# Optimization experiments

Hardware: AMD Instinct MI355X
Metric: run time of the kernel (lower is better)

## Reference

```python
import jax, jax.numpy as jnp
import numpy as np

D_MODEL = 2048
N_HEADS = 16
D_HEAD = D_MODEL // N_HEADS
SQLEN = 2048
EPS = 1e-5
XPOS_SCALE_BASE = 512.0


def apply_xpos(x, offset, inv=False):
    # x: (sqlen, d_head). Rotary embedding with xPos exponential length scaling.
    sqlen, d = x.shape
    half = d // 2
    freq = 1.0 / (10000.0 ** (jnp.arange(half, dtype=jnp.float32) / half))
    pos = jnp.arange(sqlen, dtype=jnp.float32) + offset  # absolute positions
    ang = pos[:, None] * freq[None, :]                   # (sqlen, half)
    sin, cos = jnp.sin(ang), jnp.cos(ang)
    # xPos per-dim scale zeta^(pos/scale_base); k gets the inverse scale.
    zeta = (jnp.arange(half, dtype=jnp.float32) * 2.0 + 0.4 * d) / (1.4 * d)
    sc = zeta[None, :] ** (pos[:, None] / XPOS_SCALE_BASE)
    if inv:
        sc = 1.0 / sc
    x1, x2 = x[:, :half], x[:, half:]
    r1 = (x1 * cos - x2 * sin) * sc
    r2 = (x2 * cos + x1 * sin) * sc
    return jnp.concatenate([r1, r2], axis=-1)


def group_norm(x, weight, bias):
    # x: (sqlen, d_model); n_heads groups of d_head channels each.
    xg = x.reshape(x.shape[0], N_HEADS, D_HEAD)
    mu = jnp.mean(xg, axis=-1, keepdims=True)
    var = jnp.mean((xg - mu) ** 2, axis=-1, keepdims=True)
    xn = ((xg - mu) * jax.lax.rsqrt(var + EPS)).reshape(x.shape)
    return xn * weight + bias


def setup_inputs() -> dict:
    key = jax.random.key(0)
    ks = jax.random.split(key, 9)
    s = 0.02
    return {
        "x": jax.random.normal(ks[0], (SQLEN, D_MODEL), dtype=jnp.float32),
        "state": jax.random.normal(ks[1], (N_HEADS, D_HEAD, D_HEAD), dtype=jnp.float32),
        "W_qkv": jax.random.normal(ks[2], (3 * D_MODEL, D_MODEL), dtype=jnp.float32) * s,
        "W_alpha": jax.random.normal(ks[3], (N_HEADS, D_MODEL), dtype=jnp.float32) * s,
        "b_alpha": jnp.zeros((N_HEADS,), dtype=jnp.float32),
        "alpha_base": jnp.log(jax.random.uniform(ks[4], (N_HEADS,), minval=0.95, maxval=0.999)).astype(jnp.float32),
        "gn_weight": jnp.ones((D_MODEL,), dtype=jnp.float32),
        "gn_bias": jnp.zeros((D_MODEL,), dtype=jnp.float32),
        "W_out": jax.random.normal(ks[5], (D_MODEL, D_MODEL), dtype=jnp.float32) * s,
        "W_gate": jax.random.normal(ks[6], (D_MODEL, D_MODEL), dtype=jnp.float32) * s,
        "offset": 0,
    }


def reference(x, state, W_qkv, W_alpha, b_alpha, alpha_base, gn_weight, gn_bias, W_out, W_gate, offset):
    sqlen = x.shape[0]
    # qkv projection -> (3, h, sqlen, d_head)
    qkv = (x @ W_qkv.T).reshape(sqlen, 3, N_HEADS, D_HEAD).transpose(1, 2, 0, 3)
    q, k, v = qkv[0], qkv[1], qkv[2]
    q = jax.vmap(lambda t: apply_xpos(t, offset))(q)
    k = jax.vmap(lambda t: apply_xpos(t, offset, inv=True))(k)

    # per-head, per-position decay log-rates: (h, sqlen), negative
    alphas = jax.nn.sigmoid(x @ W_alpha.T + b_alpha).T
    alphas = alpha_base[:, None] * 8.0 * alphas
    k = (1.0 - jnp.exp(alphas))[:, :, None] * k
    alphas = jnp.cumsum(alphas, axis=1)
    # causal decay matrix Delta[h,i,j] = exp(a_i - a_j) for j <= i
    Delta = jnp.tril(jnp.exp(alphas[:, :, None] - alphas[:, None, :]))

    attn = jnp.einsum('hid,hjd,hij->hij', q, k, Delta)
    ret = jnp.einsum('hij,hje->ihe', attn, v)  # (sqlen, h, d_head)

    # recurrent state carry
    new_state = jnp.exp(alphas[:, -1, None, None]) * state
    ret = ret + jnp.einsum('hid,hde,hi->ihe', q, state, jnp.exp(alphas))
    new_state = new_state + jnp.einsum('hid,hie,hi->hde', k, v, Delta[:, -1, :])

    ret = ret.reshape(sqlen, D_MODEL)
    ret = group_norm(ret, gn_weight, gn_bias)
    out = (jax.nn.swish(ret @ W_gate.T) * ret) @ W_out.T
    return (out, new_state)
```

## Files before the change

kernel.cpp:

```cpp
#include <hip/hip_runtime.h>
#include <cstddef>

#define SQLEN 2048
#define DMODEL 2048
#define NHEADS 16
#define DHEAD 128

typedef __attribute__((ext_vector_type(8))) short bf16x8;
typedef __attribute__((ext_vector_type(4))) float floatx4;

__device__ __forceinline__ unsigned short f2bf(float f) {
  union { float f; unsigned u; } c; c.f = f;
  unsigned u = c.u;
  unsigned r = u + 0x7fffu + ((u >> 16) & 1u);
  return (unsigned short)(r >> 16);
}
__device__ __forceinline__ float bf2f(unsigned short s) {
  union { unsigned u; float f; } c; c.u = ((unsigned)s) << 16;
  return c.f;
}

__global__ __launch_bounds__(256) void f2b_kernel(const float4* __restrict__ in,
                                                  ushort4* __restrict__ out) {
  int i = blockIdx.x * 256 + threadIdx.x;
  float4 v = in[i];
  ushort4 o;
  o.x = f2bf(v.x); o.y = f2bf(v.y); o.z = f2bf(v.z); o.w = f2bf(v.w);
  out[i] = o;
}

__global__ __launch_bounds__(256) void gemm_bf16_nt(const unsigned short* __restrict__ A,
                                                    const unsigned short* __restrict__ B,
                                                    float* __restrict__ C,
                                                    int M, int N, int K) {
  __shared__ __align__(16) unsigned short As[128 * 32];
  __shared__ __align__(16) unsigned short Bs[128 * 32];
  int tid = threadIdx.x;
  int wave = tid >> 6;
  int lane = tid & 63;
  int wm = wave >> 1, wn = wave & 1;
  int quad = lane >> 4, m16 = lane & 15;
  int row0 = blockIdx.y * 128, col0 = blockIdx.x * 128;

  floatx4 acc[4][4];
#pragma unroll
  for (int i = 0; i < 4; i++)
#pragma unroll
    for (int j = 0; j < 4; j++) acc[i][j] = (floatx4){0.f, 0.f, 0.f, 0.f};

  int c0 = tid, c1 = tid + 256;
  int r0c = c0 >> 2, q0c = (c0 & 3) * 8;
  int r1c = c1 >> 2, q1c = (c1 & 3) * 8;

  const size_t sK = (size_t)K;
  for (int k0 = 0; k0 < K; k0 += 32) {
    __builtin_amdgcn_global_load_lds(
        (const __attribute__((address_space(1))) unsigned int*)(A + (size_t)(row0 + r0c) * sK + k0 + q0c),
        (__attribute__((address_space(3))) unsigned int*)(As + c0 * 8), 16, 0, 0);
    __builtin_amdgcn_global_load_lds(
        (const __attribute__((address_space(1))) unsigned int*)(A + (size_t)(row0 + r1c) * sK + k0 + q1c),
        (__attribute__((address_space(3))) unsigned int*)(As + c1 * 8), 16, 0, 0);
    __builtin_amdgcn_global_load_lds(
        (const __attribute__((address_space(1))) unsigned int*)(B + (size_t)(col0 + r0c) * sK + k0 + q0c),
        (__attribute__((address_space(3))) unsigned int*)(Bs + c0 * 8), 16, 0, 0);
    __builtin_amdgcn_global_load_lds(
        (const __attribute__((address_space(1))) unsigned int*)(B + (size_t)(col0 + r1c) * sK + k0 + q1c),
        (__attribute__((address_space(3))) unsigned int*)(Bs + c1 * 8), 16, 0, 0);
    __syncthreads();

    bf16x8 af[4], bfr[4];
#pragma unroll
    for (int i = 0; i < 4; i++)
      af[i] = *(const bf16x8*)(As + (wm * 64 + i * 16 + m16) * 32 + quad * 8);
#pragma unroll
    for (int j = 0; j < 4; j++)
      bfr[j] = *(const bf16x8*)(Bs + (wn * 64 + j * 16 + m16) * 32 + quad * 8);
#pragma unroll
    for (int i = 0; i < 4; i++)
#pragma unroll
      for (int j = 0; j < 4; j++)
        acc[i][j] = __builtin_amdgcn_mfma_f32_16x16x32_bf16(af[i], bfr[j], acc[i][j], 0, 0, 0);
    __syncthreads();
  }

#pragma unroll
  for (int i = 0; i < 4; i++) {
#pragma unroll
    for (int j = 0; j < 4; j++) {
      int rr = row0 + wm * 64 + i * 16 + quad * 4;
      int cc = col0 + wn * 64 + j * 16 + m16;
#pragma unroll
      for (int r = 0; r < 4; r++)
        C[(size_t)(rr + r) * N + cc] = acc[i][j][r];
    }
  }
}

__global__ __launch_bounds__(256) void alpha_kernel(const float* __restrict__ x,
                                                    const float* __restrict__ W_alpha,
                                                    const float* __restrict__ b_alpha,
                                                    const float* __restrict__ alpha_base,
                                                    float* __restrict__ a_raw) {
  __shared__ float xs[4][2048];
  int tid = threadIdx.x;
  int t0 = blockIdx.x * 4;
#pragma unroll
  for (int p = 0; p < 8; p++) {
    int idx = tid + p * 256;
    int row = idx >> 9, c4 = idx & 511;
    *(float4*)&xs[row][c4 * 4] = *(const float4*)(x + (size_t)(t0 + row) * DMODEL + c4 * 4);
  }
  __syncthreads();
  int w = tid >> 6, lane = tid & 63;
  int t = t0 + w;
#pragma unroll
  for (int h = 0; h < NHEADS; h++) {
    const float4* wr = (const float4*)(W_alpha + (size_t)h * DMODEL);
    float s = 0.f;
#pragma unroll
    for (int i = lane; i < 512; i += 64) {
      float4 a = *(const float4*)&xs[w][i * 4];
      float4 b = wr[i];
      s += a.x * b.x + a.y * b.y + a.z * b.z + a.w * b.w;
    }
#pragma unroll
    for (int off = 32; off > 0; off >>= 1) s += __shfl_down(s, off);
    if (lane == 0) {
      float sig = 1.f / (1.f + expf(-(s + b_alpha[h])));
      a_raw[(size_t)h * SQLEN + t] = alpha_base[h] * 8.f * sig;
    }
  }
}

__global__ __launch_bounds__(256) void cumsum_kernel(const float* __restrict__ a_raw,
                                                     float* __restrict__ A) {
  int h = blockIdx.x;
  __shared__ float part[256];
  int tid = threadIdx.x;
  float v[8];
  float s = 0.f;
#pragma unroll
  for (int i = 0; i < 8; i++) {
    v[i] = a_raw[(size_t)h * SQLEN + tid * 8 + i];
    s += v[i];
  }
  part[tid] = s;
  __syncthreads();
  for (int off = 1; off < 256; off <<= 1) {
    float tmp = (tid >= off) ? part[tid - off] : 0.f;
    __syncthreads();
    part[tid] += tmp;
    __syncthreads();
  }
  float run = (tid > 0) ? part[tid - 1] : 0.f;
#pragma unroll
  for (int i = 0; i < 8; i++) {
    run += v[i];
    A[(size_t)h * SQLEN + tid * 8 + i] = run;
  }
}

__global__ __launch_bounds__(256) void xpos_kernel(const float* __restrict__ qkv,
                                                   const float* __restrict__ a_raw,
                                                   const int* __restrict__ offset_p,
                                                   unsigned short* __restrict__ qb,
                                                   unsigned short* __restrict__ kb,
                                                   unsigned short* __restrict__ vb) {
  int idx = blockIdx.x * 256 + threadIdx.x;
  int j = idx & 63;
  int t = (idx >> 6) & 2047;
  int h = idx >> 17;
  float pos = (float)(t + offset_p[0]);
  float freq = exp2f(-(float)j * (13.287712379549449f / 64.f));
  float ang = pos * freq;
  float sn = sinf(ang), cs = cosf(ang);
  float zeta = (2.f * (float)j + 51.2f) / 179.2f;
  float lzp = log2f(zeta) * pos * (1.f / 512.f);
  float sc = exp2f(lzp);
  float sci = exp2f(-lzp);
  const float* row = qkv + (size_t)t * (3 * DMODEL);
  int base = h * DHEAD + j;
  float q1 = row[base], q2 = row[base + 64];
  float k1 = row[DMODEL + base], k2 = row[DMODEL + base + 64];
  float v1 = row[2 * DMODEL + base], v2 = row[2 * DMODEL + base + 64];
  size_t o = ((size_t)h * SQLEN + t) * DHEAD + j;
  qb[o] = f2bf((q1 * cs - q2 * sn) * sc);
  qb[o + 64] = f2bf((q2 * cs + q1 * sn) * sc);
  float km = (1.f - expf(a_raw[(size_t)h * SQLEN + t])) * sci;
  kb[o] = f2bf((k1 * cs - k2 * sn) * km);
  kb[o + 64] = f2bf((k2 * cs + k1 * sn) * km);
  vb[o] = f2bf(v1);
  vb[o + 64] = f2bf(v2);
}

__global__ __launch_bounds__(256) void transpose_kv_kernel(const unsigned short* __restrict__ kb,
                                                           const unsigned short* __restrict__ vb,
                                                           const float* __restrict__ A,
                                                           unsigned short* __restrict__ kT,
                                                           unsigned short* __restrict__ vT) {
  __shared__ __align__(16) unsigned short tile[64][72];
  int h = blockIdx.z >> 1, sel = blockIdx.z & 1;
  int t0 = blockIdx.x * 64, d0 = blockIdx.y * 64;
  int tid = threadIdx.x;
  const unsigned short* src = (sel ? vb : kb) + ((size_t)h * SQLEN + t0) * DHEAD + d0;
  unsigned short* dst = (sel ? vT : kT) + (size_t)h * (DHEAD * SQLEN) + (size_t)d0 * SQLEN + t0;
  float B = A[(size_t)h * SQLEN + SQLEN - 1];
#pragma unroll
  for (int p = 0; p < 2; p++) {
    int c = tid + p * 256;
    int r = c >> 3, off = (c & 7) * 8;
    bf16x8 in = *(const bf16x8*)(src + (size_t)r * DHEAD + off);
    if (!sel) {
      float w = __expf(B - A[(size_t)h * SQLEN + t0 + r]);
      bf16x8 o;
#pragma unroll
      for (int j = 0; j < 8; j++) o[j] = (short)f2bf(bf2f((unsigned short)in[j]) * w);
      *(bf16x8*)&tile[r][off] = o;
    } else {
      *(bf16x8*)&tile[r][off] = in;
    }
  }
  __syncthreads();
#pragma unroll
  for (int p = 0; p < 2; p++) {
    int c = tid + p * 256;
    int dr = c >> 3, toff = (c & 7) * 8;
    bf16x8 o;
#pragma unroll
    for (int j = 0; j < 8; j++) o[j] = (short)tile[toff + j][dr];
    *(bf16x8*)(dst + (size_t)dr * SQLEN + toff) = o;
  }
}

__global__ __launch_bounds__(256) void transpose_state_kernel(const float* __restrict__ st,
                                                              unsigned short* __restrict__ stT) {
  __shared__ float tile[64][65];
  int h = blockIdx.z, d0 = blockIdx.x * 64, e0 = blockIdx.y * 64;
  int tid = threadIdx.x;
  const float* src = st + (size_t)h * 16384 + (size_t)d0 * DHEAD + e0;
#pragma unroll
  for (int p = 0; p < 4; p++) {
    int idx = tid + p * 256;
    int r = idx >> 4, c = (idx & 15) * 4;
    float4 f = *(const float4*)(src + (size_t)r * DHEAD + c);
    tile[r][c] = f.x; tile[r][c + 1] = f.y; tile[r][c + 2] = f.z; tile[r][c + 3] = f.w;
  }
  __syncthreads();
  unsigned short* dst = stT + (size_t)h * 16384 + (size_t)e0 * DHEAD + d0;
#pragma unroll
  for (int p = 0; p < 2; p++) {
    int idx = tid + p * 256;
    int er = idx >> 3, doff = (idx & 7) * 8;
    bf16x8 o;
#pragma unroll
    for (int j = 0; j < 8; j++) o[j] = (short)f2bf(tile[doff + j][er]);
    *(bf16x8*)(dst + (size_t)er * DHEAD + doff) = o;
  }
}

__global__ __launch_bounds__(256) void retention_mfma(const unsigned short* __restrict__ qb,
                                                      const unsigned short* __restrict__ kb,
                                                      const unsigned short* __restrict__ vT,
                                                      const unsigned short* __restrict__ stT,
                                                      const float* __restrict__ A,
                                                      float* __restrict__ ret) {
  __shared__ __align__(16) unsigned short qs[64 * 128];
  __shared__ __align__(16) unsigned short ks[64 * 128];
  __shared__ __align__(16) unsigned short vs[128 * 64];
  __shared__ __align__(16) unsigned short Ss[64 * 72];
  __shared__ float djs[64];
  int h = blockIdx.x;
  int i0 = blockIdx.y * 64;
  int tid = threadIdx.x;
  int wave = tid >> 6, lane = tid & 63, quad = lane >> 4, m16 = lane & 15;
  const float* Ah = A + (size_t)h * SQLEN;
  float c = Ah[i0];

  const unsigned short* qh = qb + ((size_t)h * SQLEN + i0) * DHEAD;
#pragma unroll
  for (int p = 0; p < 4; p++) {
    int cch = tid + p * 256;
    int r = cch >> 4, kp = (cch & 15) ^ (r & 7);
    __builtin_amdgcn_global_load_lds(
        (const __attribute__((address_space(1))) unsigned int*)(qh + (size_t)r * DHEAD + kp * 8),
        (__attribute__((address_space(3))) unsigned int*)(qs + cch * 8), 16, 0, 0);
  }
  __syncthreads();

  int rq = wave * 16 + m16;
  bf16x8 qf[4];
#pragma unroll
  for (int dc = 0; dc < 4; dc++)
    qf[dc] = *(const bf16x8*)(qs + rq * 128 + (((dc * 4 + quad) ^ (rq & 7)) * 8));
  float ei = __expf(Ah[i0 + rq] - c);

  floatx4 acc[8];
#pragma unroll
  for (int et = 0; et < 8; et++) acc[et] = (floatx4){0.f, 0.f, 0.f, 0.f};

  if (c > -87.f) {
    const unsigned short* sp = stT + (size_t)h * 16384;
    float ecr[4];
#pragma unroll
    for (int r = 0; r < 4; r++) ecr[r] = __expf(Ah[i0 + wave * 16 + quad * 4 + r]);
#pragma unroll
    for (int et = 0; et < 8; et++) {
#pragma unroll
      for (int dc = 0; dc < 4; dc++) {
        bf16x8 sf = *(const bf16x8*)(sp + (et * 16 + m16) * DHEAD + dc * 32 + quad * 8);
        acc[et] = __builtin_amdgcn_mfma_f32_16x16x32_bf16(qf[dc], sf, acc[et], 0, 0, 0);
      }
#pragma unroll
      for (int r = 0; r < 4; r++) acc[et][r] *= ecr[r];
    }
  }

  for (int j0 = 0; j0 <= i0; j0 += 64) {
    if (c - Ah[j0 + 63] < -87.f) continue;
    __syncthreads();
    const unsigned short* kh = kb + ((size_t)h * SQLEN + j0) * DHEAD;
    const unsigned short* vh = vT + (size_t)h * (DHEAD * SQLEN) + j0;
#pragma unroll
    for (int p = 0; p < 4; p++) {
      int cch = tid + p * 256;
      int r = cch >> 4, kp = (cch & 15) ^ (r & 7);
      __builtin_amdgcn_global_load_lds(
          (const __attribute__((address_space(1))) unsigned int*)(kh + (size_t)r * DHEAD + kp * 8),
          (__attribute__((address_space(3))) unsigned int*)(ks + cch * 8), 16, 0, 0);
      int e = cch >> 3, tp = (cch & 7) ^ (e & 7);
      __builtin_amdgcn_global_load_lds(
          (const __attribute__((address_space(1))) unsigned int*)(vh + (size_t)e * SQLEN + tp * 8),
          (__attribute__((address_space(3))) unsigned int*)(vs + cch * 8), 16, 0, 0);
    }
    if (tid < 64) djs[tid] = __expf(c - Ah[j0 + tid]);
    __syncthreads();

    bool diag = (j0 == i0);
    int ii = rq;
#pragma unroll
    for (int jt = 0; jt < 4; jt++) {
      floatx4 s = (floatx4){0.f, 0.f, 0.f, 0.f};
#pragma unroll
      for (int dc = 0; dc < 4; dc++) {
        int rk = jt * 16 + m16;
        bf16x8 kf = *(const bf16x8*)(ks + rk * 128 + (((dc * 4 + quad) ^ (rk & 7)) * 8));
        s = __builtin_amdgcn_mfma_f32_16x16x32_bf16(kf, qf[dc], s, 0, 0, 0);
      }
      int jb = jt * 16 + quad * 4;
      float4 dj4 = *(const float4*)&djs[jb];
      ushort4 pk;
      pk.x = f2bf((diag && (jb + 0 > ii)) ? 0.f : s[0] * ei * dj4.x);
      pk.y = f2bf((diag && (jb + 1 > ii)) ? 0.f : s[1] * ei * dj4.y);
      pk.z = f2bf((diag && (jb + 2 > ii)) ? 0.f : s[2] * ei * dj4.z);
      pk.w = f2bf((diag && (jb + 3 > ii)) ? 0.f : s[3] * ei * dj4.w);
      *(ushort4*)(Ss + rq * 72 + jb) = pk;
    }

    bf16x8 sfr[2];
#pragma unroll
    for (int kc = 0; kc < 2; kc++)
      sfr[kc] = *(const bf16x8*)(Ss + rq * 72 + kc * 32 + quad * 8);
#pragma unroll
    for (int et = 0; et < 8; et++) {
#pragma unroll
      for (int kc = 0; kc < 2; kc++) {
        int e = et * 16 + m16;
        bf16x8 vf = *(const bf16x8*)(vs + e * 64 + (((kc * 4 + quad) ^ (e & 7)) * 8));
        acc[et] = __builtin_amdgcn_mfma_f32_16x16x32_bf16(sfr[kc], vf, acc[et], 0, 0, 0);
      }
    }
  }

#pragma unroll
  for (int et = 0; et < 8; et++) {
    int col = h * DHEAD + et * 16 + m16;
#pragma unroll
    for (int r = 0; r < 4; r++) {
      int row = i0 + wave * 16 + quad * 4 + r;
      ret[(size_t)row * DMODEL + col] = acc[et][r];
    }
  }
}

__global__ __launch_bounds__(256) void state_gemm(const unsigned short* __restrict__ kT,
                                                  const unsigned short* __restrict__ vT,
                                                  float* __restrict__ P) {
  __shared__ __align__(16) unsigned short As[128 * 32];
  __shared__ __align__(16) unsigned short Bs[128 * 32];
  int chunk = blockIdx.x, h = blockIdx.y;
  int tid = threadIdx.x;
  int wave = tid >> 6, lane = tid & 63;
  int wm = wave >> 1, wn = wave & 1;
  int quad = lane >> 4, m16 = lane & 15;
  const unsigned short* Ab = kT + (size_t)h * (DHEAD * SQLEN);
  const unsigned short* Bb = vT + (size_t)h * (DHEAD * SQLEN);

  floatx4 acc[4][4];
#pragma unroll
  for (int i = 0; i < 4; i++)
#pragma unroll
    for (int j = 0; j < 4; j++) acc[i][j] = (floatx4){0.f, 0.f, 0.f, 0.f};

  int c0 = tid, c1 = tid + 256;
  int r0c = c0 >> 2, q0c = (c0 & 3) * 8;
  int r1c = c1 >> 2, q1c = (c1 & 3) * 8;

  for (int k0 = chunk * 256; k0 < chunk * 256 + 256; k0 += 32) {
    __builtin_amdgcn_global_load_lds(
        (const __attribute__((address_space(1))) unsigned int*)(Ab + (size_t)r0c * SQLEN + k0 + q0c),
        (__attribute__((address_space(3))) unsigned int*)(As + c0 * 8), 16, 0, 0);
    __builtin_amdgcn_global_load_lds(
        (const __attribute__((address_space(1))) unsigned int*)(Ab + (size_t)r1c * SQLEN + k0 + q1c),
        (__attribute__((address_space(3))) unsigned int*)(As + c1 * 8), 16, 0, 0);
    __builtin_amdgcn_global_load_lds(
        (const __attribute__((address_space(1))) unsigned int*)(Bb + (size_t)r0c * SQLEN + k0 + q0c),
        (__attribute__((address_space(3))) unsigned int*)(Bs + c0 * 8), 16, 0, 0);
    __builtin_amdgcn_global_load_lds(
        (const __attribute__((address_space(1))) unsigned int*)(Bb + (size_t)r1c * SQLEN + k0 + q1c),
        (__attribute__((address_space(3))) unsigned int*)(Bs + c1 * 8), 16, 0, 0);
    __syncthreads();

    bf16x8 af[4], bfr[4];
#pragma unroll
    for (int i = 0; i < 4; i++)
      af[i] = *(const bf16x8*)(As + (wm * 64 + i * 16 + m16) * 32 + quad * 8);
#pragma unroll
    for (int j = 0; j < 4; j++)
      bfr[j] = *(const bf16x8*)(Bs + (wn * 64 + j * 16 + m16) * 32 + quad * 8);
#pragma unroll
    for (int i = 0; i < 4; i++)
#pragma unroll
      for (int j = 0; j < 4; j++)
        acc[i][j] = __builtin_amdgcn_mfma_f32_16x16x32_bf16(af[i], bfr[j], acc[i][j], 0, 0, 0);
    __syncthreads();
  }

  float* Pp = P + (size_t)(h * 8 + chunk) * 16384;
#pragma unroll
  for (int i = 0; i < 4; i++)
#pragma unroll
    for (int j = 0; j < 4; j++) {
      int rr = wm * 64 + i * 16 + quad * 4;
      int cc = wn * 64 + j * 16 + m16;
#pragma unroll
      for (int r = 0; r < 4; r++)
        Pp[(size_t)(rr + r) * DHEAD + cc] = acc[i][j][r];
    }
}

__global__ __launch_bounds__(256) void state_combine(const float* __restrict__ P,
                                                     const float* __restrict__ state,
                                                     const float* __restrict__ A,
                                                     float* __restrict__ out_state) {
  int idx = blockIdx.x * 256 + threadIdx.x;
  int h = idx >> 14;
  int de = idx & 16383;
  float B = A[(size_t)h * SQLEN + SQLEN - 1];
  float s = __expf(B) * state[idx];
#pragma unroll
  for (int c = 0; c < 8; c++) s += P[(size_t)(h * 8 + c) * 16384 + de];
  out_state[idx] = s;
}

__global__ __launch_bounds__(256) void groupnorm_kernel(const float* __restrict__ ret,
                                                        const float* __restrict__ w,
                                                        const float* __restrict__ b,
                                                        float* __restrict__ out,
                                                        unsigned short* __restrict__ outb) {
  int gw = blockIdx.x * 4 + (threadIdx.x >> 6);
  int lane = threadIdx.x & 63;
  int t = gw >> 4, h = gw & 15;
  const float* p = ret + (size_t)t * DMODEL + h * DHEAD;
  float x0 = p[lane], x1 = p[lane + 64];
  float s = x0 + x1, ss = x0 * x0 + x1 * x1;
#pragma unroll
  for (int off = 32; off > 0; off >>= 1) {
    s += __shfl_xor(s, off);
    ss += __shfl_xor(ss, off);
  }
  float mu = s * (1.f / 128.f);
  float var = ss * (1.f / 128.f) - mu * mu;
  float inv = rsqrtf(var + 1e-5f);
  int cidx = h * DHEAD + lane;
  float r0 = (x0 - mu) * inv * w[cidx] + b[cidx];
  float r1 = (x1 - mu) * inv * w[cidx + 64] + b[cidx + 64];
  size_t o = (size_t)t * DMODEL;
  out[o + cidx] = r0;
  out[o + cidx + 64] = r1;
  outb[o + cidx] = f2bf(r0);
  outb[o + cidx + 64] = f2bf(r1);
}

__global__ __launch_bounds__(256) void swishmul_kernel(const float* __restrict__ G,
                                                       const float* __restrict__ rn,
                                                       ushort4* __restrict__ Hb) {
  int i = blockIdx.x * 256 + threadIdx.x;
  float4 g = ((const float4*)G)[i];
  float4 r = ((const float4*)rn)[i];
  ushort4 o;
  o.x = f2bf(g.x / (1.f + expf(-g.x)) * r.x);
  o.y = f2bf(g.y / (1.f + expf(-g.y)) * r.y);
  o.z = f2bf(g.z / (1.f + expf(-g.z)) * r.z);
  o.w = f2bf(g.w / (1.f + expf(-g.w)) * r.w);
  Hb[i] = o;
}

extern "C" void kernel_launch(void* const* d_in, const int* in_sizes, int n_in,
                              void* d_out, int out_size, void* d_ws, size_t ws_size,
                              hipStream_t stream) {
  const float* x = (const float*)d_in[0];
  const float* state = (const float*)d_in[1];
  const float* W_qkv = (const float*)d_in[2];
  const float* W_alpha = (const float*)d_in[3];
  const float* b_alpha = (const float*)d_in[4];
  const float* alpha_base = (const float*)d_in[5];
  const float* gn_w = (const float*)d_in[6];
  const float* gn_b = (const float*)d_in[7];
  const float* W_out = (const float*)d_in[8];
  const float* W_gate = (const float*)d_in[9];
  const int* offset = (const int*)d_in[10];

  float* ws = (float*)d_ws;
  float* qkv = ws;
  float* G   = ws;
  float* P   = ws + 4194304;
  float* ret = ws + 25165824;
  float* rn  = ws + 29360128;
  float* araw = ws + 33554432;
  float* Acum = ws + 33587200;

  unsigned short* xb    = (unsigned short*)(ws + 12582912);
  unsigned short* Wqkvb = (unsigned short*)(ws + 16777216);
  unsigned short* qb    = (unsigned short*)(ws + 12582912);
  unsigned short* kb    = (unsigned short*)(ws + 14680064);
  unsigned short* vb    = (unsigned short*)(ws + 16777216);
  unsigned short* kT_s  = (unsigned short*)(ws + 18874368);
  unsigned short* vT_b  = (unsigned short*)(ws + 20971520);
  unsigned short* stT_b = (unsigned short*)(ws + 23068672);
  unsigned short* rnb    = (unsigned short*)(ws + 12582912);
  unsigned short* Wgateb = (unsigned short*)(ws + 14680064);
  unsigned short* Woutb  = (unsigned short*)(ws + 16777216);
  unsigned short* Hb     = (unsigned short*)(ws + 18874368);

  float* out = (float*)d_out;
  float* out_state = out + 4194304;

  dim3 blk(256);
  f2b_kernel<<<dim3(4096), blk, 0, stream>>>((const float4*)x, (ushort4*)xb);
  f2b_kernel<<<dim3(12288), blk, 0, stream>>>((const float4*)W_qkv, (ushort4*)Wqkvb);
  gemm_bf16_nt<<<dim3(48, 16), blk, 0, stream>>>(xb, Wqkvb, qkv, 2048, 6144, 2048);

  alpha_kernel<<<dim3(512), blk, 0, stream>>>(x, W_alpha, b_alpha, alpha_base, araw);
  cumsum_kernel<<<dim3(16), blk, 0, stream>>>(araw, Acum);
  xpos_kernel<<<dim3(8192), blk, 0, stream>>>(qkv, araw, offset, qb, kb, vb);
  transpose_kv_kernel<<<dim3(32, 2, 32), blk, 0, stream>>>(kb, vb, Acum, kT_s, vT_b);
  transpose_state_kernel<<<dim3(2, 2, 16), blk, 0, stream>>>(state, stT_b);

  retention_mfma<<<dim3(16, 32), blk, 0, stream>>>(qb, kb, vT_b, stT_b, Acum, ret);
  state_gemm<<<dim3(8, 16), blk, 0, stream>>>(kT_s, vT_b, P);
  state_combine<<<dim3(1024), blk, 0, stream>>>(P, state, Acum, out_state);
  groupnorm_kernel<<<dim3(8192), blk, 0, stream>>>(ret, gn_w, gn_b, rn, rnb);

  f2b_kernel<<<dim3(4096), blk, 0, stream>>>((const float4*)W_gate, (ushort4*)Wgateb);
  f2b_kernel<<<dim3(4096), blk, 0, stream>>>((const float4*)W_out, (ushort4*)Woutb);
  gemm_bf16_nt<<<dim3(16, 16), blk, 0, stream>>>(rnb, Wgateb, G, 2048, 2048, 2048);
  swishmul_kernel<<<dim3(4096), blk, 0, stream>>>(G, rn, (ushort4*)Hb);
  gemm_bf16_nt<<<dim3(16, 16), blk, 0, stream>>>(Hb, Woutb, out, 2048, 2048, 2048);
}
```

Measured before the change: 449.7 us.

## Fuse groupnorm into retention epilogue and swish-mul into gate GEMM

Group normalization now runs in the retention kernel's epilogue using cross-lane shuffles, so the intermediate ret buffer and the separate groupnorm kernel go away. The gate GEMM applies swish times rn in its epilogue and writes bf16 Hb directly, which removes the G round trip and the swishmul kernel. The two weight conversions are merged into one launch. Q fragments are loaded straight from global memory instead of staged through LDS, and several transcendentals switch to fast intrinsics, which costs some accuracy.

Result: faster. 436.0 us (-3.0%).

```diff
diff --git a/kernel.cpp b/kernel.cpp
--- a/kernel.cpp
+++ b/kernel.cpp
@@ -29,6 +29,21 @@
   out[i] = o;
 }
 
+__global__ __launch_bounds__(256) void f2b2_kernel(const float4* __restrict__ in0,
+                                                   ushort4* __restrict__ out0,
+                                                   const float4* __restrict__ in1,
+                                                   ushort4* __restrict__ out1,
+                                                   int half_blocks) {
+  int b = blockIdx.x;
+  const float4* in = (b < half_blocks) ? in0 : in1;
+  ushort4* out = (b < half_blocks) ? out0 : out1;
+  int i = (b < half_blocks ? b : b - half_blocks) * 256 + threadIdx.x;
+  float4 v = in[i];
+  ushort4 o;
+  o.x = f2bf(v.x); o.y = f2bf(v.y); o.z = f2bf(v.z); o.w = f2bf(v.w);
+  out[i] = o;
+}
+
 __global__ __launch_bounds__(256) void gemm_bf16_nt(const unsigned short* __restrict__ A,
                                                     const unsigned short* __restrict__ B,
                                                     float* __restrict__ C,
@@ -96,6 +111,78 @@
   }
 }
 
+__global__ __launch_bounds__(256) void gemm_swish_nt(const unsigned short* __restrict__ A,
+                                                     const unsigned short* __restrict__ B,
+                                                     const float* __restrict__ rn,
+                                                     unsigned short* __restrict__ Hb,
+                                                     int M, int N, int K) {
+  __shared__ __align__(16) unsigned short As[128 * 32];
+  __shared__ __align__(16) unsigned short Bs[128 * 32];
+  int tid = threadIdx.x;
+  int wave = tid >> 6;
+  int lane = tid & 63;
+  int wm = wave >> 1, wn = wave & 1;
+  int quad = lane >> 4, m16 = lane & 15;
+  int row0 = blockIdx.y * 128, col0 = blockIdx.x * 128;
+
+  floatx4 acc[4][4];
+#pragma unroll
+  for (int i = 0; i < 4; i++)
+#pragma unroll
+    for (int j = 0; j < 4; j++) acc[i][j] = (floatx4){0.f, 0.f, 0.f, 0.f};
+
+  int c0 = tid, c1 = tid + 256;
+  int r0c = c0 >> 2, q0c = (c0 & 3) * 8;
+  int r1c = c1 >> 2, q1c = (c1 & 3) * 8;
+
+  const size_t sK = (size_t)K;
+  for (int k0 = 0; k0 < K; k0 += 32) {
+    __builtin_amdgcn_global_load_lds(
+        (const __attribute__((address_space(1))) unsigned int*)(A + (size_t)(row0 + r0c) * sK + k0 + q0c),
+        (__attribute__((address_space(3))) unsigned int*)(As + c0 * 8), 16, 0, 0);
+    __builtin_amdgcn_global_load_lds(
+        (const __attribute__((address_space(1))) unsigned int*)(A + (size_t)(row0 + r1c) * sK + k0 + q1c),
+        (__attribute__((address_space(3))) unsigned int*)(As + c1 * 8), 16, 0, 0);
+    __builtin_amdgcn_global_load_lds(
+        (const __attribute__((address_space(1))) unsigned int*)(B + (size_t)(col0 + r0c) * sK + k0 + q0c),
+        (__attribute__((address_space(3))) unsigned int*)(Bs + c0 * 8), 16, 0, 0);
+    __builtin_amdgcn_global_load_lds(
+        (const __attribute__((address_space(1))) unsigned int*)(B + (size_t)(col0 + r1c) * sK + k0 + q1c),
+        (__attribute__((address_space(3))) unsigned int*)(Bs + c1 * 8), 16, 0, 0);
+    __syncthreads();
+
+    bf16x8 af[4], bfr[4];
+#pragma unroll
+    for (int i = 0; i < 4; i++)
+      af[i] = *(const bf16x8*)(As + (wm * 64 + i * 16 + m16) * 32 + quad * 8);
+#pragma unroll
+    for (int j = 0; j < 4; j++)
+      bfr[j] = *(const bf16x8*)(Bs + (wn * 64 + j * 16 + m16) * 32 + quad * 8);
+#pragma unroll
+    for (int i = 0; i < 4; i++)
+#pragma unroll
+      for (int j = 0; j < 4; j++)
+        acc[i][j] = __builtin_amdgcn_mfma_f32_16x16x32_bf16(af[i], bfr[j], acc[i][j], 0, 0, 0);
+    __syncthreads();
+  }
+
+#pragma unroll
+  for (int i = 0; i < 4; i++) {
+#pragma unroll
+    for (int j = 0; j < 4; j++) {
+      int rr = row0 + wm * 64 + i * 16 + quad * 4;
+      int cc = col0 + wn * 64 + j * 16 + m16;
+#pragma unroll
+      for (int r = 0; r < 4; r++) {
+        float g = acc[i][j][r];
+        float rv = rn[(size_t)(rr + r) * N + cc];
+        float hh = g / (1.f + __expf(-g)) * rv;
+        Hb[(size_t)(rr + r) * N + cc] = f2bf(hh);
+      }
+    }
+  }
+}
+
 __global__ __launch_bounds__(256) void alpha_kernel(const float* __restrict__ x,
                                                     const float* __restrict__ W_alpha,
                                                     const float* __restrict__ b_alpha,
@@ -126,7 +213,7 @@
 #pragma unroll
     for (int off = 32; off > 0; off >>= 1) s += __shfl_down(s, off);
     if (lane == 0) {
-      float sig = 1.f / (1.f + expf(-(s + b_alpha[h])));
+      float sig = 1.f / (1.f + __expf(-(s + b_alpha[h])));
       a_raw[(size_t)h * SQLEN + t] = alpha_base[h] * 8.f * sig;
     }
   }
@@ -173,9 +260,9 @@
   float pos = (float)(t + offset_p[0]);
   float freq = exp2f(-(float)j * (13.287712379549449f / 64.f));
   float ang = pos * freq;
-  float sn = sinf(ang), cs = cosf(ang);
+  float sn = __sinf(ang), cs = __cosf(ang);
   float zeta = (2.f * (float)j + 51.2f) / 179.2f;
-  float lzp = log2f(zeta) * pos * (1.f / 512.f);
+  float lzp = __log2f(zeta) * pos * (1.f / 512.f);
   float sc = exp2f(lzp);
   float sci = exp2f(-lzp);
   const float* row = qkv + (size_t)t * (3 * DMODEL);
@@ -186,7 +273,7 @@
   size_t o = ((size_t)h * SQLEN + t) * DHEAD + j;
   qb[o] = f2bf((q1 * cs - q2 * sn) * sc);
   qb[o + 64] = f2bf((q2 * cs + q1 * sn) * sc);
-  float km = (1.f - expf(a_raw[(size_t)h * SQLEN + t])) * sci;
+  float km = (1.f - __expf(a_raw[(size_t)h * SQLEN + t])) * sci;
   kb[o] = f2bf((k1 * cs - k2 * sn) * km);
   kb[o + 64] = f2bf((k2 * cs + k1 * sn) * km);
   vb[o] = f2bf(v1);
@@ -263,8 +350,10 @@
                                                       const unsigned short* __restrict__ vT,
                                                       const unsigned short* __restrict__ stT,
                                                       const float* __restrict__ A,
-                                                      float* __restrict__ ret) {
-  __shared__ __align__(16) unsigned short qs[64 * 128];
+                                                      const float* __restrict__ gn_w,
+                                                      const float* __restrict__ gn_b,
+                                                      float* __restrict__ rn,
+                                                      unsigned short* __restrict__ rnb) {
   __shared__ __align__(16) unsigned short ks[64 * 128];
   __shared__ __align__(16) unsigned short vs[128 * 64];
   __shared__ __align__(16) unsigned short Ss[64 * 72];
@@ -275,24 +364,22 @@
   int wave = tid >> 6, lane = tid & 63, quad = lane >> 4, m16 = lane & 15;
   const float* Ah = A + (size_t)h * SQLEN;
   float c = Ah[i0];
-
-  const unsigned short* qh = qb + ((size_t)h * SQLEN + i0) * DHEAD;
-#pragma unroll
-  for (int p = 0; p < 4; p++) {
-    int cch = tid + p * 256;
-    int r = cch >> 4, kp = (cch & 15) ^ (r & 7);
-    __builtin_amdgcn_global_load_lds(
-        (const __attribute__((address_space(1))) unsigned int*)(qh + (size_t)r * DHEAD + kp * 8),
-        (__attribute__((address_space(3))) unsigned int*)(qs + cch * 8), 16, 0, 0);
-  }
-  __syncthreads();
-
   int rq = wave * 16 + m16;
+
+  const unsigned short* qh = qb + ((size_t)h * SQLEN + i0 + rq) * DHEAD;
   bf16x8 qf[4];
 #pragma unroll
   for (int dc = 0; dc < 4; dc++)
-    qf[dc] = *(const bf16x8*)(qs + rq * 128 + (((dc * 4 + quad) ^ (rq & 7)) * 8));
+    qf[dc] = *(const bf16x8*)(qh + dc * 32 + quad * 8);
   float ei = __expf(Ah[i0 + rq] - c);
+
+  float wg[8], bg[8];
+#pragma unroll
+  for (int et = 0; et < 8; et++) {
+    int col = h * DHEAD + et * 16 + m16;
+    wg[et] = gn_w[col];
+    bg[et] = gn_b[col];
+  }
 
   floatx4 acc[8];
 #pragma unroll
@@ -336,7 +423,6 @@
     __syncthreads();
 
     bool diag = (j0 == i0);
-    int ii = rq;
 #pragma unroll
     for (int jt = 0; jt < 4; jt++) {
       floatx4 s = (floatx4){0.f, 0.f, 0.f, 0.f};
@@ -349,10 +435,10 @@
       int jb = jt * 16 + quad * 4;
       float4 dj4 = *(const float4*)&djs[jb];
       ushort4 pk;
-      pk.x = f2bf((diag && (jb + 0 > ii)) ? 0.f : s[0] * ei * dj4.x);
-      pk.y = f2bf((diag && (jb + 1 > ii)) ? 0.f : s[1] * ei * dj4.y);
-      pk.z = f2bf((diag && (jb + 2 > ii)) ? 0.f : s[2] * ei * dj4.z);
-      pk.w = f2bf((diag && (jb + 3 > ii)) ? 0.f : s[3] * ei * dj4.w);
+      pk.x = f2bf((diag && (jb + 0 > rq)) ? 0.f : s[0] * ei * dj4.x);
+      pk.y = f2bf((diag && (jb + 1 > rq)) ? 0.f : s[1] * ei * dj4.y);
+      pk.z = f2bf((diag && (jb + 2 > rq)) ? 0.f : s[2] * ei * dj4.z);
+      pk.w = f2bf((diag && (jb + 3 > rq)) ? 0.f : s[3] * ei * dj4.w);
       *(ushort4*)(Ss + rq * 72 + jb) = pk;
     }
 
@@ -372,12 +458,28 @@
   }
 
 #pragma unroll
-  for (int et = 0; et < 8; et++) {
-    int col = h * DHEAD + et * 16 + m16;
-#pragma unroll
-    for (int r = 0; r < 4; r++) {
-      int row = i0 + wave * 16 + quad * 4 + r;
-      ret[(size_t)row * DMODEL + col] = acc[et][r];
+  for (int r = 0; r < 4; r++) {
+    float s = 0.f, ss = 0.f;
+#pragma unroll
+    for (int et = 0; et < 8; et++) {
+      float v = acc[et][r];
+      s += v; ss += v * v;
+    }
+#pragma unroll
+    for (int off = 8; off > 0; off >>= 1) {
+      s += __shfl_xor(s, off);
+      ss += __shfl_xor(ss, off);
+    }
+    float mu = s * (1.f / 128.f);
+    float var = ss * (1.f / 128.f) - mu * mu;
+    float inv = rsqrtf(var + 1e-5f);
+    int row = i0 + wave * 16 + quad * 4 + r;
+    size_t o = (size_t)row * DMODEL + h * DHEAD;
+#pragma unroll
+    for (int et = 0; et < 8; et++) {
+      float rv = (acc[et][r] - mu) * inv * wg[et] + bg[et];
+      rn[o + et * 16 + m16] = rv;
+      rnb[o + et * 16 + m16] = f2bf(rv);
     }
   }
 }
@@ -460,49 +562,6 @@
 #pragma unroll
   for (int c = 0; c < 8; c++) s += P[(size_t)(h * 8 + c) * 16384 + de];
   out_state[idx] = s;
-}
-
-__global__ __launch_bounds__(256) void groupnorm_kernel(const float* __restrict__ ret,
-                                                        const float* __restrict__ w,
-                                                        const float* __restrict__ b,
-                                                        float* __restrict__ out,
-                                                        unsigned short* __restrict__ outb) {
-  int gw = blockIdx.x * 4 + (threadIdx.x >> 6);
-  int lane = threadIdx.x & 63;
-  int t = gw >> 4, h = gw & 15;
-  const float* p = ret + (size_t)t * DMODEL + h * DHEAD;
-  float x0 = p[lane], x1 = p[lane + 64];
-  float s = x0 + x1, ss = x0 * x0 + x1 * x1;
-#pragma unroll
-  for (int off = 32; off > 0; off >>= 1) {
-    s += __shfl_xor(s, off);
-    ss += __shfl_xor(ss, off);
-  }
-  float mu = s * (1.f / 128.f);
-  float var = ss * (1.f / 128.f) - mu * mu;
-  float inv = rsqrtf(var + 1e-5f);
-  int cidx = h * DHEAD + lane;
-  float r0 = (x0 - mu) * inv * w[cidx] + b[cidx];
-  float r1 = (x1 - mu) * inv * w[cidx + 64] + b[cidx + 64];
-  size_t o = (size_t)t * DMODEL;
-  out[o + cidx] = r0;
-  out[o + cidx + 64] = r1;
-  outb[o + cidx] = f2bf(r0);
-  outb[o + cidx + 64] = f2bf(r1);
-}
-
-__global__ __launch_bounds__(256) void swishmul_kernel(const float* __restrict__ G,
-                                                       const float* __restrict__ rn,
-                                                       ushort4* __restrict__ Hb) {
-  int i = blockIdx.x * 256 + threadIdx.x;
-  float4 g = ((const float4*)G)[i];
-  float4 r = ((const float4*)rn)[i];
-  ushort4 o;
-  o.x = f2bf(g.x / (1.f + expf(-g.x)) * r.x);
-  o.y = f2bf(g.y / (1.f + expf(-g.y)) * r.y);
-  o.z = f2bf(g.z / (1.f + expf(-g.z)) * r.z);
-  o.w = f2bf(g.w / (1.f + expf(-g.w)) * r.w);
-  Hb[i] = o;
 }
 
 extern "C" void kernel_launch(void* const* d_in, const int* in_sizes, int n_in,
@@ -522,9 +581,7 @@
 
   float* ws = (float*)d_ws;
   float* qkv = ws;
-  float* G   = ws;
   float* P   = ws + 4194304;
-  float* ret = ws + 25165824;
   float* rn  = ws + 29360128;
   float* araw = ws + 33554432;
   float* Acum = ws + 33587200;
@@ -537,7 +594,7 @@
   unsigned short* kT_s  = (unsigned short*)(ws + 18874368);
   unsigned short* vT_b  = (unsigned short*)(ws + 20971520);
   unsigned short* stT_b = (unsigned short*)(ws + 23068672);
-  unsigned short* rnb    = (unsigned short*)(ws + 12582912);
+  unsigned short* rnb   = (unsigned short*)(ws + 25165824);
   unsigned short* Wgateb = (unsigned short*)(ws + 14680064);
   unsigned short* Woutb  = (unsigned short*)(ws + 16777216);
   unsigned short* Hb     = (unsigned short*)(ws + 18874368);
@@ -556,14 +613,13 @@
   transpose_kv_kernel<<<dim3(32, 2, 32), blk, 0, stream>>>(kb, vb, Acum, kT_s, vT_b);
   transpose_state_kernel<<<dim3(2, 2, 16), blk, 0, stream>>>(state, stT_b);
 
-  retention_mfma<<<dim3(16, 32), blk, 0, stream>>>(qb, kb, vT_b, stT_b, Acum, ret);
+  retention_mfma<<<dim3(16, 32), blk, 0, stream>>>(qb, kb, vT_b, stT_b, Acum,
+                                                   gn_w, gn_b, rn, rnb);
   state_gemm<<<dim3(8, 16), blk, 0, stream>>>(kT_s, vT_b, P);
   state_combine<<<dim3(1024), blk, 0, stream>>>(P, state, Acum, out_state);
-  groupnorm_kernel<<<dim3(8192), blk, 0, stream>>>(ret, gn_w, gn_b, rn, rnb);
-
-  f2b_kernel<<<dim3(4096), blk, 0, stream>>>((const float4*)W_gate, (ushort4*)Wgateb);
-  f2b_kernel<<<dim3(4096), blk, 0, stream>>>((const float4*)W_out, (ushort4*)Woutb);
-  gemm_bf16_nt<<<dim3(16, 16), blk, 0, stream>>>(rnb, Wgateb, G, 2048, 2048, 2048);
-  swishmul_kernel<<<dim3(4096), blk, 0, stream>>>(G, rn, (ushort4*)Hb);
+
+  f2b2_kernel<<<dim3(8192), blk, 0, stream>>>((const float4*)W_gate, (ushort4*)Wgateb,
+                                              (const float4*)W_out, (ushort4*)Woutb, 4096);
+  gemm_swish_nt<<<dim3(16, 16), blk, 0, stream>>>(rnb, Wgateb, rn, Hb, 2048, 2048, 2048);
   gemm_bf16_nt<<<dim3(16, 16), blk, 0, stream>>>(Hb, Woutb, out, 2048, 2048, 2048);
 }
```
